# Performance work log

Hardware: AMD Instinct MI355X
Metric: run time of the kernel (lower is better)

Reference implementation:

```python
import jax, jax.numpy as jnp
import numpy as np


def setup_inputs() -> dict:
    key = jax.random.key(0)
    ks = jax.random.split(key, 12)
    N_DRUGS, D, N_CELLS, C_IN, E = 4096, 128, 1024, 1000, 500000
    inp = {
        "drug_hidden_out": jax.random.normal(ks[0], (N_DRUGS, D), dtype=jnp.float32),
        "cell_hidden_out": jax.random.normal(ks[1], (N_CELLS, C_IN), dtype=jnp.float32),
        # columns: drug1_idx, drug2_idx, cell_idx, label (original code indexes
        # drug_hidden_out with ALL THREE index columns, so bound by N_DRUGS)
        "all_edges": jax.random.randint(ks[2], (E, 4), 0, N_DRUGS, dtype=jnp.int64),
        # proj: Linear(1000, 128)
        "proj_W": jax.random.normal(ks[3], (D, C_IN), dtype=jnp.float32) * 0.03,
        "proj_b": jnp.zeros((D,), dtype=jnp.float32),
        # NN: Linear(128,32) -> ReLU -> Linear(32,32) -> ReLU -> Linear(32,32)
        #     -> ReLU -> Dropout(eval=identity) -> Linear(32,1) -> Sigmoid
        "W1": jax.random.normal(ks[4], (32, D), dtype=jnp.float32) * 0.08,
        "b1": jnp.zeros((32,), dtype=jnp.float32),
        "W2": jax.random.normal(ks[5], (32, 32), dtype=jnp.float32) * 0.17,
        "b2": jnp.zeros((32,), dtype=jnp.float32),
        "W3": jax.random.normal(ks[6], (32, 32), dtype=jnp.float32) * 0.17,
        "b3": jnp.zeros((32,), dtype=jnp.float32),
        "W4": jax.random.normal(ks[7], (1, 32), dtype=jnp.float32) * 0.17,
        "b4": jnp.zeros((1,), dtype=jnp.float32),
    }
    return inp


def reference(drug_hidden_out, cell_hidden_out, all_edges,
              proj_W, proj_b, W1, b1, W2, b2, W3, b3, W4, b4):
    # proj is computed in the original forward but its result is never used
    # downstream (the code re-indexes drug_hidden_out for cell_fea).
    _cell_proj = cell_hidden_out @ proj_W.T + proj_b  # [n_cells, 128], dead value

    edges = all_edges.T                 # [4, E]
    label = edges[3]                    # [E]
    edge_index = edges[:3]              # [3, E]

    drug1_fea = drug_hidden_out[edge_index[0]]   # [E, 128] gather
    drug2_fea = drug_hidden_out[edge_index[1]]   # [E, 128] gather
    cell_fea = drug_hidden_out[edge_index[2]]    # [E, 128] gather (faithful to source bug)
    logits = drug1_fea * drug2_fea * cell_fea    # [E, 128]

    h = jax.nn.relu(logits @ W1.T + b1)          # [E, 32]
    h = jax.nn.relu(h @ W2.T + b2)               # [E, 32]
    h = jax.nn.relu(h @ W3.T + b3)               # [E, 32] (dropout = identity in eval)
    x = jax.nn.sigmoid(h @ W4.T + b4)            # [E, 1]
    return x, label
```

## Files before the change

### kernel.cpp

```cpp
#include <hip/hip_runtime.h>
#include <stdint.h>

#define DD 128
#define HH 32
#define RS 40
#define TABQ (4096 * DD / 4)
#define BLOB_OFF (1u << 20)

typedef _Float16 f16;
typedef _Float16 f16x4 __attribute__((ext_vector_type(4)));
typedef _Float16 f16x8 __attribute__((ext_vector_type(8)));
typedef float    f32x4 __attribute__((ext_vector_type(4)));

#define GL1(p)  ((const __attribute__((address_space(1))) void*)(p))
#define LDS3(p) ((__attribute__((address_space(3))) void*)(p))

__global__ __launch_bounds__(256)
void synergy_prepass(const float* __restrict__ drug, const int* __restrict__ edges,
                     const float* __restrict__ W1, const float* __restrict__ W2,
                     const float* __restrict__ W3,
                     f16* __restrict__ tab, float* __restrict__ out, int E, int wBlock)
{
    const int tid = threadIdx.x;
    if ((int)blockIdx.x == wBlock) {
        f16x8* __restrict__ blob16 = (f16x8*)((char*)tab + BLOB_OFF);
        const float4* __restrict__ W1v = (const float4*)W1;
        #pragma unroll
        for (int p = 0; p < 2; ++p) {
            const int S = p * 256 + tid;
            const int t = S >> 8, f = (S >> 6) & 3, l = S & 63;
            const int mm = l & 15, qq = l >> 4;
            const int c4 = (t * 16 + mm) * (DD / 4) + f * 8 + qq * 2;
            const float4 w0 = W1v[c4], w1 = W1v[c4 + 1];
            f16x8 r;
            r[0]=(f16)w0.x; r[1]=(f16)w0.y; r[2]=(f16)w0.z; r[3]=(f16)w0.w;
            r[4]=(f16)w1.x; r[5]=(f16)w1.y; r[6]=(f16)w1.z; r[7]=(f16)w1.w;
            blob16[S] = r;
        }
        {
            const int B = tid & 127;
            const int t = B >> 6, l = B & 63;
            const int mm = l & 15, qq = l >> 4;
            const int c4 = (t * 16 + mm) * (HH / 4) + qq * 2;
            const float4* __restrict__ src = (tid < 128) ? (const float4*)W2 : (const float4*)W3;
            const float4 w0 = src[c4], w1 = src[c4 + 1];
            f16x8 r;
            r[0]=(f16)w0.x; r[1]=(f16)w0.y; r[2]=(f16)w0.z; r[3]=(f16)w0.w;
            r[4]=(f16)w1.x; r[5]=(f16)w1.y; r[6]=(f16)w1.z; r[7]=(f16)w1.w;
            blob16[512 + (tid & 128) + B] = r;
        }
        return;
    }
    const int i = blockIdx.x * 256 + tid;
    if (i < TABQ) {
        const float4 v = ((const float4*)drug)[i];
        f16x4 h;
        h[0]=(f16)v.x; h[1]=(f16)v.y; h[2]=(f16)v.z; h[3]=(f16)v.w;
        ((f16x4*)tab)[i] = h;
    }
    if (i < E) out[E + i] = (float)edges[4 * i + 3];
}

__global__ __launch_bounds__(256, 2)
void synergy_main(const f16* __restrict__ tab, const int* __restrict__ edges,
                  const float* __restrict__ W4, const float* __restrict__ b1,
                  const float* __restrict__ b2, const float* __restrict__ b3,
                  const float* __restrict__ b4, float* __restrict__ out, int E)
{
    __shared__ __align__(16) f16 wblob[6144];
    __shared__ __align__(16) f16 stage[4][6144];

    const int tid  = threadIdx.x;
    const int wave = tid >> 6;
    const int lane = tid & 63;
    const int m    = lane & 15;
    const int q    = lane >> 4;

    const int waveBase = blockIdx.x * 64 + wave * 16;

    int idx[12];
    #pragma unroll
    for (int s = 0; s < 12; ++s) {
        const int t = s >> 2, g = s & 3;
        int e = waveBase + 4 * g + q;
        e = (e < E) ? e : (E - 1);
        idx[s] = edges[e * 4 + t];
    }
    const float b1a = b1[m], b1b = b1[16 + m];
    const float b2a = b2[m], b2b = b2[16 + m];
    const float b3a = b3[m], b3b = b3[16 + m];
    const float w4a = W4[m], w4b = W4[16 + m];
    const float b4v = b4[0];

    const char* __restrict__ tabB = (const char*)tab;
    for (int s = wave; s < 12; s += 4)
        __builtin_amdgcn_global_load_lds(GL1(tabB + BLOB_OFF + s * 1024 + lane * 16),
                                         LDS3((char*)wblob + s * 1024), 16, 0, 0);
    __syncthreads();

    const f16x8* __restrict__ blobL = (const f16x8*)wblob;
    f16x8 wa[2][4];
    #pragma unroll
    for (int t = 0; t < 2; ++t)
        #pragma unroll
        for (int f = 0; f < 4; ++f)
            wa[t][f] = blobL[(t * 4 + f) * 64 + lane];

    f16* __restrict__ stg = stage[wave];
    #pragma unroll
    for (int s = 0; s < 12; ++s) {
        const int t = s >> 2, g = s & 3;
        const int e_t = 4 * g + q;
        const int seg = (m + e_t) & 15;
        __builtin_amdgcn_global_load_lds(GL1(tabB + (size_t)((idx[s] << 8) + (seg << 4))),
                                         LDS3((char*)stg + (t * 16 + 4 * g) * 256), 16, 0, 0);
    }
    __builtin_amdgcn_sched_barrier(0);
    __builtin_amdgcn_s_waitcnt(0x0F70);
    __builtin_amdgcn_sched_barrier(0);

    f32x4 acc0 = {b1a, b1a, b1a, b1a};
    f32x4 acc1 = {b1b, b1b, b1b, b1b};
    #pragma unroll
    for (int f = 0; f < 4; ++f) {
        const int slot = (((f * 4 + q) - m) & 15) << 3;
        const f16x8 v0 = *(const f16x8*)(stg + (0 * 16 + m) * 128 + slot);
        const f16x8 v1 = *(const f16x8*)(stg + (1 * 16 + m) * 128 + slot);
        const f16x8 v2 = *(const f16x8*)(stg + (2 * 16 + m) * 128 + slot);
        const f16x8 p = v0 * v1 * v2;
        acc0 = __builtin_amdgcn_mfma_f32_16x16x32_f16(p, wa[0][f], acc0, 0, 0, 0);
        acc1 = __builtin_amdgcn_mfma_f32_16x16x32_f16(p, wa[1][f], acc1, 0, 0, 0);
    }
    f16* __restrict__ hb = stg;
    #pragma unroll
    for (int r = 0; r < 4; ++r) {
        const int row = 4 * q + r;
        hb[row * RS + m]      = (f16)fmaxf(acc0[r], 0.0f);
        hb[row * RS + 16 + m] = (f16)fmaxf(acc1[r], 0.0f);
    }

    const f16x8 w2a = blobL[512 + lane], w2b = blobL[576 + lane];
    const f16x8 a2 = *(const f16x8*)(hb + m * RS + q * 8);
    f32x4 c0 = {b2a, b2a, b2a, b2a};
    f32x4 c1 = {b2b, b2b, b2b, b2b};
    c0 = __builtin_amdgcn_mfma_f32_16x16x32_f16(a2, w2a, c0, 0, 0, 0);
    c1 = __builtin_amdgcn_mfma_f32_16x16x32_f16(a2, w2b, c1, 0, 0, 0);
    #pragma unroll
    for (int r = 0; r < 4; ++r) {
        const int row = 4 * q + r;
        hb[row * RS + m]      = (f16)fmaxf(c0[r], 0.0f);
        hb[row * RS + 16 + m] = (f16)fmaxf(c1[r], 0.0f);
    }

    const f16x8 w3a = blobL[640 + lane], w3b = blobL[704 + lane];
    const f16x8 a3 = *(const f16x8*)(hb + m * RS + q * 8);
    f32x4 d0 = {b3a, b3a, b3a, b3a};
    f32x4 d1 = {b3b, b3b, b3b, b3b};
    d0 = __builtin_amdgcn_mfma_f32_16x16x32_f16(a3, w3a, d0, 0, 0, 0);
    d1 = __builtin_amdgcn_mfma_f32_16x16x32_f16(a3, w3b, d1, 0, 0, 0);

    float zr[4];
    #pragma unroll
    for (int r = 0; r < 4; ++r)
        zr[r] = fmaxf(d0[r], 0.0f) * w4a + fmaxf(d1[r], 0.0f) * w4b;
    #pragma unroll
    for (int dd = 1; dd < 16; dd <<= 1)
        #pragma unroll
        for (int r = 0; r < 4; ++r)
            zr[r] += __shfl_xor(zr[r], dd, 64);
    if (m == 0) {
        #pragma unroll
        for (int r = 0; r < 4; ++r) {
            const int e = waveBase + 4 * q + r;
            if (e < E) out[e] = 1.0f / (1.0f + __expf(-(zr[r] + b4v)));
        }
    }
}

extern "C" void kernel_launch(void* const* d_in, const int* in_sizes, int n_in,
                              void* d_out, int out_size, void* d_ws, size_t ws_size,
                              hipStream_t stream)
{
    const float* drug  = (const float*)d_in[0];
    const int*   edges = (const int*)d_in[2];
    const float* W1 = (const float*)d_in[5];
    const float* b1 = (const float*)d_in[6];
    const float* W2 = (const float*)d_in[7];
    const float* b2 = (const float*)d_in[8];
    const float* W3 = (const float*)d_in[9];
    const float* b3 = (const float*)d_in[10];
    const float* W4 = (const float*)d_in[11];
    const float* b4 = (const float*)d_in[12];
    float* out = (float*)d_out;
    f16*   tab = (f16*)d_ws;

    const int E = in_sizes[2] / 4;

    const int labelBlocks = (E + 255) / 256;
    hipLaunchKernelGGL(synergy_prepass, dim3(labelBlocks + 1), dim3(256), 0, stream,
                       drug, edges, W1, W2, W3, tab, out, E, labelBlocks);
    hipLaunchKernelGGL(synergy_main, dim3((E + 63) / 64), dim3(256), 0, stream,
                       tab, edges, W4, b1, b2, b3, b4, out, E);
}
```

Measured before the change: 135.9 us.

## Move label copy into main kernel, load edges as int4 and weights from global

The prepass now only converts the drug table and weight blob, using a fixed 513 blocks instead of one block per 256 edges. The main kernel does the label copy itself. Each lane loads a whole edge row as one int4 and the indices are shared across lanes with shuffles, replacing twelve scalar gathers. Weights are read straight from global into registers, which drops the LDS weight staging and the block-wide barrier, and occupancy is raised to 3 blocks per SIMD. This removes a large share of the prepass traffic and the serialising barrier, but adds register pressure and repeated global weight reads per wave.

```diff
diff --git a/kernel.cpp b/kernel.cpp
--- a/kernel.cpp
+++ b/kernel.cpp
@@ -16,13 +16,12 @@
 #define LDS3(p) ((__attribute__((address_space(3))) void*)(p))
 
 __global__ __launch_bounds__(256)
-void synergy_prepass(const float* __restrict__ drug, const int* __restrict__ edges,
+void synergy_prepass(const float* __restrict__ drug,
                      const float* __restrict__ W1, const float* __restrict__ W2,
-                     const float* __restrict__ W3,
-                     f16* __restrict__ tab, float* __restrict__ out, int E, int wBlock)
+                     const float* __restrict__ W3, f16* __restrict__ tab)
 {
     const int tid = threadIdx.x;
-    if ((int)blockIdx.x == wBlock) {
+    if ((int)blockIdx.x == 512) {
         f16x8* __restrict__ blob16 = (f16x8*)((char*)tab + BLOB_OFF);
         const float4* __restrict__ W1v = (const float4*)W1;
         #pragma unroll
@@ -58,16 +57,14 @@
         h[0]=(f16)v.x; h[1]=(f16)v.y; h[2]=(f16)v.z; h[3]=(f16)v.w;
         ((f16x4*)tab)[i] = h;
     }
-    if (i < E) out[E + i] = (float)edges[4 * i + 3];
 }
 
-__global__ __launch_bounds__(256, 2)
+__global__ __launch_bounds__(256, 3)
 void synergy_main(const f16* __restrict__ tab, const int* __restrict__ edges,
                   const float* __restrict__ W4, const float* __restrict__ b1,
                   const float* __restrict__ b2, const float* __restrict__ b3,
                   const float* __restrict__ b4, float* __restrict__ out, int E)
 {
-    __shared__ __align__(16) f16 wblob[6144];
     __shared__ __align__(16) f16 stage[4][6144];
 
     const int tid  = threadIdx.x;
@@ -77,44 +74,49 @@
     const int q    = lane >> 4;
 
     const int waveBase = blockIdx.x * 64 + wave * 16;
-
-    int idx[12];
-    #pragma unroll
-    for (int s = 0; s < 12; ++s) {
-        const int t = s >> 2, g = s & 3;
-        int e = waveBase + 4 * g + q;
-        e = (e < E) ? e : (E - 1);
-        idx[s] = edges[e * 4 + t];
-    }
+    const char* __restrict__ tabB = (const char*)tab;
+
+    const f16x8* __restrict__ blobG = (const f16x8*)(tabB + BLOB_OFF);
+    f16x8 wa[2][4];
+    #pragma unroll
+    for (int t = 0; t < 2; ++t)
+        #pragma unroll
+        for (int f = 0; f < 4; ++f)
+            wa[t][f] = blobG[(t * 4 + f) * 64 + lane];
+    const f16x8 w2a = blobG[512 + lane], w2b = blobG[576 + lane];
+    const f16x8 w3a = blobG[640 + lane], w3b = blobG[704 + lane];
     const float b1a = b1[m], b1b = b1[16 + m];
     const float b2a = b2[m], b2b = b2[16 + m];
     const float b3a = b3[m], b3b = b3[16 + m];
     const float w4a = W4[m], w4b = W4[16 + m];
     const float b4v = b4[0];
 
-    const char* __restrict__ tabB = (const char*)tab;
-    for (int s = wave; s < 12; s += 4)
-        __builtin_amdgcn_global_load_lds(GL1(tabB + BLOB_OFF + s * 1024 + lane * 16),
-                                         LDS3((char*)wblob + s * 1024), 16, 0, 0);
-    __syncthreads();
-
-    const f16x8* __restrict__ blobL = (const f16x8*)wblob;
-    f16x8 wa[2][4];
-    #pragma unroll
-    for (int t = 0; t < 2; ++t)
-        #pragma unroll
-        for (int f = 0; f < 4; ++f)
-            wa[t][f] = blobL[(t * 4 + f) * 64 + lane];
+    int eL = waveBase + m;
+    eL = (eL < E) ? eL : (E - 1);
+    const int4 ed = ((const int4*)edges)[eL];
+
+    if (lane < 16 && waveBase + lane < E)
+        out[E + waveBase + lane] = (float)ed.w;
+
+    int rowb[12];
+    #pragma unroll
+    for (int g = 0; g < 4; ++g) {
+        const int src = 4 * g + q;
+        rowb[0 * 4 + g] = __shfl(ed.x, src, 64) << 8;
+        rowb[1 * 4 + g] = __shfl(ed.y, src, 64) << 8;
+        rowb[2 * 4 + g] = __shfl(ed.z, src, 64) << 8;
+    }
 
     f16* __restrict__ stg = stage[wave];
     #pragma unroll
-    for (int s = 0; s < 12; ++s) {
-        const int t = s >> 2, g = s & 3;
-        const int e_t = 4 * g + q;
-        const int seg = (m + e_t) & 15;
-        __builtin_amdgcn_global_load_lds(GL1(tabB + (size_t)((idx[s] << 8) + (seg << 4))),
-                                         LDS3((char*)stg + (t * 16 + 4 * g) * 256), 16, 0, 0);
-    }
+    for (int t = 0; t < 3; ++t)
+        #pragma unroll
+        for (int g = 0; g < 4; ++g) {
+            const int seg = (m + 4 * g + q) & 15;
+            __builtin_amdgcn_global_load_lds(
+                GL1(tabB + (size_t)(rowb[t * 4 + g] + (seg << 4))),
+                LDS3((char*)stg + (t * 16 + 4 * g) * 256), 16, 0, 0);
+        }
     __builtin_amdgcn_sched_barrier(0);
     __builtin_amdgcn_s_waitcnt(0x0F70);
     __builtin_amdgcn_sched_barrier(0);
@@ -139,7 +141,6 @@
         hb[row * RS + 16 + m] = (f16)fmaxf(acc1[r], 0.0f);
     }
 
-    const f16x8 w2a = blobL[512 + lane], w2b = blobL[576 + lane];
     const f16x8 a2 = *(const f16x8*)(hb + m * RS + q * 8);
     f32x4 c0 = {b2a, b2a, b2a, b2a};
     f32x4 c1 = {b2b, b2b, b2b, b2b};
@@ -152,7 +153,6 @@
         hb[row * RS + 16 + m] = (f16)fmaxf(c1[r], 0.0f);
     }
 
-    const f16x8 w3a = blobL[640 + lane], w3b = blobL[704 + lane];
     const f16x8 a3 = *(const f16x8*)(hb + m * RS + q * 8);
     f32x4 d0 = {b3a, b3a, b3a, b3a};
     f32x4 d1 = {b3b, b3b, b3b, b3b};
@@ -196,9 +196,8 @@
 
     const int E = in_sizes[2] / 4;
 
-    const int labelBlocks = (E + 255) / 256;
-    hipLaunchKernelGGL(synergy_prepass, dim3(labelBlocks + 1), dim3(256), 0, stream,
-                       drug, edges, W1, W2, W3, tab, out, E, labelBlocks);
+    hipLaunchKernelGGL(synergy_prepass, dim3(513), dim3(256), 0, stream,
+                       drug, W1, W2, W3, tab);
     hipLaunchKernelGGL(synergy_main, dim3((E + 63) / 64), dim3(256), 0, stream,
                        tab, edges, W4, b1, b2, b3, b4, out, E);
 }
```

Result: faster. 125.9 us (-7.4%).
